# Optimization experiments

Measured on AMD Instinct MI355X. Metric: run time of the kernel, lower is better.

The kernel has to match this reference:

```python
import jax, jax.numpy as jnp
import numpy as np

N_NODES = 50000
N_EDGES = 800000
IN_DIM_N = 256
IN_DIM_E = 64
OUT_DIM_N = 64
OUT_DIM_E = 64


def setup_inputs() -> dict:
    key = jax.random.key(0)
    ks = jax.random.split(key, 8)
    nfeats = jax.random.normal(ks[0], (N_NODES, IN_DIM_N), dtype=jnp.float32)
    efeats = jax.random.normal(ks[1], (N_EDGES, IN_DIM_E), dtype=jnp.float32)
    src = jax.random.randint(ks[2], (N_EDGES,), 0, N_NODES)
    dst = jax.random.randint(ks[3], (N_EDGES,), 0, N_NODES)
    # xavier-style scaled weights
    W_fc = jax.random.normal(ks[4], (OUT_DIM_N, IN_DIM_N), dtype=jnp.float32) * (2.0 / (OUT_DIM_N + IN_DIM_N)) ** 0.5
    cat_dim = IN_DIM_E + 2 * OUT_DIM_N  # 192
    W_e = jax.random.normal(ks[5], (OUT_DIM_E, cat_dim), dtype=jnp.float32) * (2.0 / (OUT_DIM_E + cat_dim)) ** 0.5
    b_e = jnp.zeros((OUT_DIM_E,), dtype=jnp.float32)
    w_c = jax.random.normal(ks[6], (1, OUT_DIM_E), dtype=jnp.float32) * (2.0 / (1 + OUT_DIM_E)) ** 0.5
    return {"nfeats": nfeats, "efeats": efeats, "src": src, "dst": dst,
            "W_fc": W_fc, "W_e": W_e, "b_e": b_e, "w_c": w_c}


def reference(nfeats, efeats, src, dst, W_fc, W_e, b_e, w_c):
    N = nfeats.shape[0]
    # node projection (no bias)
    z = nfeats @ W_fc.T                                   # [N, out_n]
    # edge attention MLP on [z_src | efeat | z_dst]
    stacked = jnp.concatenate([z[src], efeats, z[dst]], axis=1)  # [E, in_e + 2*out_n]
    feat_e = jax.nn.leaky_relu(stacked @ W_e.T + b_e)     # [E, out_e], slope 0.01 = torch default
    a = (feat_e @ w_c.T)[:, 0]                            # [E]
    # segment softmax over incoming edges of each dst node
    m = jax.ops.segment_max(a, dst, num_segments=N)       # [N] (-inf for empty segs, never gathered)
    ex = jnp.exp(a - m[dst])                              # [E]
    s = jax.ops.segment_sum(ex, dst, num_segments=N)      # [N]
    alpha = ex / s[dst]                                   # [E]
    # weighted scatter-sum aggregate of source z
    h = jax.ops.segment_sum(alpha[:, None] * z[src], dst, num_segments=N)  # [N, out_n]
    return h, feat_e
```

## Files before the change

kernel.cpp:

```cpp
#include <hip/hip_runtime.h>
#include <hip/hip_bf16.h>

#define N_NODES 50000
#define N_EDGES 800000
#define IN_N    256
#define D       64

typedef __attribute__((ext_vector_type(8))) short short8;
typedef __attribute__((ext_vector_type(4))) float f32x4;

__device__ __forceinline__ float bf2f(unsigned short h) {
    union { unsigned int u; float f; } x; x.u = ((unsigned int)h) << 16; return x.f;
}
__device__ __forceinline__ unsigned short f2bf(float f) {
    union { float f; unsigned int u; } x; x.f = f;
    unsigned int r = x.u + 0x7fff + ((x.u >> 16) & 1);
    return (unsigned short)(r >> 16);
}
__device__ __forceinline__ short8 pack8(f32x4 p0, f32x4 p1) {
    short8 r;
    r[0] = (short)f2bf(p0[0]); r[1] = (short)f2bf(p0[1]);
    r[2] = (short)f2bf(p0[2]); r[3] = (short)f2bf(p0[3]);
    r[4] = (short)f2bf(p1[0]); r[5] = (short)f2bf(p1[1]);
    r[6] = (short)f2bf(p1[2]); r[7] = (short)f2bf(p1[3]);
    return r;
}

__global__ void count_kernel(const int* __restrict__ dst, int* __restrict__ count) {
    int i = blockIdx.x * blockDim.x + threadIdx.x;
    int stride = gridDim.x * blockDim.x;
    for (; i < N_EDGES / 4; i += stride) {
        int4 d = ((const int4*)dst)[i];
        atomicAdd(&count[d.x], 1);
        atomicAdd(&count[d.y], 1);
        atomicAdd(&count[d.z], 1);
        atomicAdd(&count[d.w], 1);
    }
}

__global__ __launch_bounds__(1024) void scan_kernel(const int* __restrict__ count,
                                                    int* __restrict__ offsets,
                                                    int* __restrict__ cursor) {
    __shared__ int part[1024];
    const int t = threadIdx.x;
    const int C = (N_NODES + 1023) / 1024;
    const int base = t * C;
    int s = 0;
    for (int i = 0; i < C; ++i) {
        int idx = base + i;
        if (idx < N_NODES) s += count[idx];
    }
    part[t] = s;
    __syncthreads();
    for (int st = 1; st < 1024; st <<= 1) {
        int v = (t >= st) ? part[t - st] : 0;
        __syncthreads();
        part[t] += v;
        __syncthreads();
    }
    int run = part[t] - s;
    for (int i = 0; i < C; ++i) {
        int idx = base + i;
        if (idx < N_NODES) {
            offsets[idx] = run;
            cursor[idx]  = run;
            run += count[idx];
        }
    }
    if (t == 1023) offsets[N_NODES] = part[1023];
}

__global__ void prep_kernel(const float* __restrict__ W_fc, const float* __restrict__ W_e,
                            unsigned short* __restrict__ Wz,
                            unsigned short* __restrict__ Wu,
                            unsigned short* __restrict__ Wv)
{
    int flat = blockIdx.x * blockDim.x + threadIdx.x;
    if (flat >= 3 * 64 * 256) return;
    int mat = flat >> 14;
    int idx = flat & 16383;
    if (mat == 0) {
        Wz[idx] = f2bf(W_fc[idx]);
        return;
    }
    int o = idx >> 8, i = idx & 255;
    const float* wrow = W_e + (size_t)o * 192 + (mat == 2 ? 128 : 0);
    float s = 0.f;
    #pragma unroll 8
    for (int j = 0; j < 64; ++j) s += wrow[j] * W_fc[(size_t)j * 256 + i];
    (mat == 1 ? Wu : Wv)[idx] = f2bf(s);
}

__global__ __launch_bounds__(256) void node_kernel(
    const float* __restrict__ nf,
    const unsigned short* __restrict__ Wz, const unsigned short* __restrict__ Wu,
    const unsigned short* __restrict__ Wv, const float* __restrict__ b_e,
    unsigned short* __restrict__ z_bf, unsigned short* __restrict__ u_bf,
    unsigned short* __restrict__ v_bf)
{
    const int lanelo = threadIdx.x & 15, quad = (threadIdx.x >> 4) & 3;
    float bias[4];
    #pragma unroll
    for (int t = 0; t < 4; ++t) bias[t] = b_e[t * 16 + lanelo];
    const int wflat = blockIdx.x * 4 + (threadIdx.x >> 6);
    const int nw = gridDim.x * 4;
    const f32x4 z4 = {0.f, 0.f, 0.f, 0.f};
    for (int g = wflat; g < N_NODES / 16; g += nw) {
        const int n0 = g * 16;
        f32x4 az[4] = {z4, z4, z4, z4};
        f32x4 au[4] = {z4, z4, z4, z4};
        f32x4 av[4] = {z4, z4, z4, z4};
        const float* arow = nf + (size_t)(n0 + lanelo) * IN_N;
        #pragma unroll
        for (int h = 0; h < 8; ++h) {
            const float* ap = arow + h * 32 + quad * 8;
            f32x4 p0 = *(const f32x4*)ap;
            f32x4 p1 = *(const f32x4*)(ap + 4);
            short8 a = pack8(p0, p1);
            const int bo = h * 32 + quad * 8;
            #pragma unroll
            for (int t = 0; t < 4; ++t) {
                const size_t rb = (size_t)(t * 16 + lanelo) * 256 + bo;
                az[t] = __builtin_amdgcn_mfma_f32_16x16x32_bf16(a, *(const short8*)&Wz[rb], az[t], 0, 0, 0);
                au[t] = __builtin_amdgcn_mfma_f32_16x16x32_bf16(a, *(const short8*)&Wu[rb], au[t], 0, 0, 0);
                av[t] = __builtin_amdgcn_mfma_f32_16x16x32_bf16(a, *(const short8*)&Wv[rb], av[t], 0, 0, 0);
            }
        }
        #pragma unroll
        for (int t = 0; t < 4; ++t)
            #pragma unroll
            for (int r = 0; r < 4; ++r) {
                const size_t row = (size_t)(n0 + quad * 4 + r) * D + t * 16 + lanelo;
                z_bf[row] = f2bf(az[t][r]);
                u_bf[row] = f2bf(au[t][r] + bias[t]);
                v_bf[row] = f2bf(av[t][r]);
            }
    }
}

__global__ __launch_bounds__(256) void edge_kernel(
    const float* __restrict__ efeats,
    const int* __restrict__ src, const int* __restrict__ dst,
    const float* __restrict__ W_e, const float* __restrict__ w_c,
    const unsigned short* __restrict__ u_bf, const unsigned short* __restrict__ v_bf,
    int* __restrict__ cursor, unsigned long long* __restrict__ csr,
    float* __restrict__ feat_out)
{
    const int lanelo = threadIdx.x & 15, quad = (threadIdx.x >> 4) & 3;
    short8 b2[4][2];
    #pragma unroll
    for (int t = 0; t < 4; ++t)
        #pragma unroll
        for (int h = 0; h < 2; ++h)
            #pragma unroll
            for (int j = 0; j < 8; ++j)
                b2[t][h][j] = (short)f2bf(W_e[(size_t)(t * 16 + lanelo) * 192 + 64 + h * 32 + quad * 8 + j]);
    float wcv[4];
    #pragma unroll
    for (int t = 0; t < 4; ++t) wcv[t] = w_c[t * 16 + lanelo];

    const int wflat = blockIdx.x * 4 + (threadIdx.x >> 6);
    const int nw = gridDim.x * 4;
    const f32x4 z4 = {0.f, 0.f, 0.f, 0.f};
    for (int g = wflat; g < N_EDGES / 16; g += nw) {
        const int e0 = g * 16;
        f32x4 acc[4] = {z4, z4, z4, z4};
        const float* ar = efeats + (size_t)(e0 + lanelo) * D;
        #pragma unroll
        for (int h = 0; h < 2; ++h) {
            f32x4 p0 = __builtin_nontemporal_load((const f32x4*)(ar + h * 32 + quad * 8));
            f32x4 p1 = __builtin_nontemporal_load((const f32x4*)(ar + h * 32 + quad * 8 + 4));
            short8 a = pack8(p0, p1);
            #pragma unroll
            for (int t = 0; t < 4; ++t)
                acc[t] = __builtin_amdgcn_mfma_f32_16x16x32_bf16(a, b2[t][h], acc[t], 0, 0, 0);
        }
        int sn[4], dn[4];
        #pragma unroll
        for (int r = 0; r < 4; ++r) {
            sn[r] = src[e0 + quad * 4 + r];
            dn[r] = dst[e0 + quad * 4 + r];
        }
        float part[4];
        #pragma unroll
        for (int r = 0; r < 4; ++r) {
            float p = 0.f;
            #pragma unroll
            for (int t = 0; t < 4; ++t) {
                float f = acc[t][r]
                        + bf2f(u_bf[(size_t)sn[r] * D + t * 16 + lanelo])
                        + bf2f(v_bf[(size_t)dn[r] * D + t * 16 + lanelo]);
                f = f > 0.f ? f : 0.01f * f;
                __builtin_nontemporal_store(f, &feat_out[(size_t)(e0 + quad * 4 + r) * D + t * 16 + lanelo]);
                p += f * wcv[t];
            }
            part[r] = p;
        }
        #pragma unroll
        for (int st = 1; st < 16; st <<= 1) {
            #pragma unroll
            for (int r = 0; r < 4; ++r) part[r] += __shfl_xor(part[r], st, 64);
        }
        #pragma unroll
        for (int r = 0; r < 4; ++r) {
            float ex = __expf(part[r]);
            if (lanelo == 0) {
                int pos = atomicAdd(&cursor[dn[r]], 1);
                csr[pos] = ((unsigned long long)__float_as_uint(ex) << 32)
                         | (unsigned long long)(unsigned int)sn[r];
            }
        }
    }
}

__global__ __launch_bounds__(256) void agg_kernel(
    const unsigned long long* __restrict__ csr,
    const int* __restrict__ offsets,
    const unsigned short* __restrict__ z_bf,
    float* __restrict__ h)
{
    const int lane = threadIdx.x & 63;
    const int wid = (blockIdx.x * blockDim.x + threadIdx.x) >> 6;
    const int nw = (gridDim.x * blockDim.x) >> 6;
    for (int n = wid; n < N_NODES; n += nw) {
        const int off = offsets[n];
        const int d = offsets[n + 1] - off;
        float acc = 0.f, ssum = 0.f;
        for (int base = 0; base < d; base += 64) {
            const int cnt = min(d - base, 64);
            unsigned long long pk = csr[off + base + min(lane, cnt - 1)];
            unsigned int hi = (unsigned int)(pk >> 32);
            unsigned int lo = (unsigned int)pk;
            int j = 0;
            for (; j + 4 <= cnt; j += 4) {
                float x0 = __uint_as_float(__shfl((int)hi, j,     64));
                float x1 = __uint_as_float(__shfl((int)hi, j + 1, 64));
                float x2 = __uint_as_float(__shfl((int)hi, j + 2, 64));
                float x3 = __uint_as_float(__shfl((int)hi, j + 3, 64));
                int s0 = __shfl((int)lo, j,     64);
                int s1 = __shfl((int)lo, j + 1, 64);
                int s2 = __shfl((int)lo, j + 2, 64);
                int s3 = __shfl((int)lo, j + 3, 64);
                float z0 = bf2f(z_bf[(size_t)s0 * D + lane]);
                float z1 = bf2f(z_bf[(size_t)s1 * D + lane]);
                float z2 = bf2f(z_bf[(size_t)s2 * D + lane]);
                float z3 = bf2f(z_bf[(size_t)s3 * D + lane]);
                acc += x0 * z0; acc += x1 * z1; acc += x2 * z2; acc += x3 * z3;
                ssum += (x0 + x1) + (x2 + x3);
            }
            for (; j < cnt; ++j) {
                float xj = __uint_as_float(__shfl((int)hi, j, 64));
                int sj = __shfl((int)lo, j, 64);
                acc += xj * bf2f(z_bf[(size_t)sj * D + lane]);
                ssum += xj;
            }
        }
        h[(size_t)n * D + lane] = ssum > 0.f ? acc / ssum : 0.f;
    }
}

extern "C" void kernel_launch(void* const* d_in, const int* in_sizes, int n_in,
                              void* d_out, int out_size, void* d_ws, size_t ws_size,
                              hipStream_t stream)
{
    const float* nfeats = (const float*)d_in[0];
    const float* efeats = (const float*)d_in[1];
    const int* src = (const int*)d_in[2];
    const int* dst = (const int*)d_in[3];
    const float* W_fc = (const float*)d_in[4];
    const float* W_e  = (const float*)d_in[5];
    const float* b_e  = (const float*)d_in[6];
    const float* w_c  = (const float*)d_in[7];

    unsigned short* z_bf = (unsigned short*)d_ws;
    unsigned short* u_bf = z_bf + (size_t)N_NODES * D;
    unsigned short* v_bf = u_bf + (size_t)N_NODES * D;
    unsigned long long* csr = (unsigned long long*)(v_bf + (size_t)N_NODES * D);
    unsigned short* Wz = (unsigned short*)(csr + (size_t)N_EDGES);
    unsigned short* Wu = Wz + 64 * 256;
    unsigned short* Wv = Wu + 64 * 256;
    int* count   = (int*)(Wv + 64 * 256);
    int* offsets = count + N_NODES;
    int* cursor  = offsets + N_NODES + 1;

    float* h_out = (float*)d_out;
    float* f_out = h_out + (size_t)N_NODES * D;

    hipMemsetAsync(count, 0, N_NODES * sizeof(int), stream);
    count_kernel<<<512, 256, 0, stream>>>(dst, count);
    scan_kernel<<<1, 1024, 0, stream>>>(count, offsets, cursor);
    prep_kernel<<<192, 256, 0, stream>>>(W_fc, W_e, Wz, Wu, Wv);
    node_kernel<<<782, 256, 0, stream>>>(nfeats, Wz, Wu, Wv, b_e, z_bf, u_bf, v_bf);
    edge_kernel<<<2048, 256, 0, stream>>>(efeats, src, dst, W_e, w_c, u_bf, v_bf,
                                          cursor, csr, f_out);
    agg_kernel<<<2048, 256, 0, stream>>>(csr, offsets, z_bf, h_out);
}
```

Baseline: 722.3 us.

## Fuse all phases into one cooperative persistent kernel with grid syncs

Replaces the memset and six separate kernel launches with a single cooperative kernel of 1024 blocks that runs zeroing, weight prep, degree count, a hierarchical three-stage scan, node projection, edge MLP, and aggregation, separated by grid-wide barriers. The single-block scan becomes a chunked parallel scan, and the end-exclusive cursor produced by the edge scatter now supplies segment bounds, so the offsets array is gone. The aggregation loop no longer cooperatively loads the CSR into lanes and broadcasts it with shuffles; every lane loads each CSR entry directly, unrolled by eight. The goal is to remove launch gaps and the serial scan. The trade-off is grid-sync overhead, a fixed grid size for every phase, and extra redundant CSR loads in aggregation.

```diff
diff --git a/kernel.cpp b/kernel.cpp
--- a/kernel.cpp
+++ b/kernel.cpp
@@ -1,10 +1,16 @@
 #include <hip/hip_runtime.h>
 #include <hip/hip_bf16.h>
+#include <hip/hip_cooperative_groups.h>
+
+namespace cg = cooperative_groups;
 
 #define N_NODES 50000
 #define N_EDGES 800000
 #define IN_N    256
 #define D       64
+#define NBLK    1024
+#define NTHR    256
+#define NCHUNK  1021
 
 typedef __attribute__((ext_vector_type(8))) short short8;
 typedef __attribute__((ext_vector_type(4))) float f32x4;
@@ -26,10 +32,29 @@
     return r;
 }
 
-__global__ void count_kernel(const int* __restrict__ dst, int* __restrict__ count) {
-    int i = blockIdx.x * blockDim.x + threadIdx.x;
-    int stride = gridDim.x * blockDim.x;
-    for (; i < N_EDGES / 4; i += stride) {
+
+__device__ __forceinline__ void ph_zero_prep(int gtid, int gsz,
+    const float* __restrict__ W_fc, const float* __restrict__ W_e,
+    unsigned short* __restrict__ Wz, unsigned short* __restrict__ Wu,
+    unsigned short* __restrict__ Wv, int* __restrict__ count)
+{
+    for (int i = gtid; i < N_NODES; i += gsz) count[i] = 0;
+    for (int f = gtid; f < 3 * 64 * 256; f += gsz) {
+        int mat = f >> 14, idx = f & 16383;
+        if (mat == 0) { Wz[idx] = f2bf(W_fc[idx]); continue; }
+        int o = idx >> 8, i = idx & 255;
+        const float* wrow = W_e + (size_t)o * 192 + (mat == 2 ? 128 : 0);
+        float s = 0.f;
+        #pragma unroll 8
+        for (int j = 0; j < 64; ++j) s += wrow[j] * W_fc[(size_t)j * 256 + i];
+        (mat == 1 ? Wu : Wv)[idx] = f2bf(s);
+    }
+}
+
+__device__ __forceinline__ void ph_count(int gtid, int gsz,
+    const int* __restrict__ dst, int* __restrict__ count)
+{
+    for (int i = gtid; i < N_EDGES / 4; i += gsz) {
         int4 d = ((const int4*)dst)[i];
         atomicAdd(&count[d.x], 1);
         atomicAdd(&count[d.y], 1);
@@ -38,74 +63,69 @@
     }
 }
 
-__global__ __launch_bounds__(1024) void scan_kernel(const int* __restrict__ count,
-                                                    int* __restrict__ offsets,
-                                                    int* __restrict__ cursor) {
-    __shared__ int part[1024];
-    const int t = threadIdx.x;
-    const int C = (N_NODES + 1023) / 1024;
-    const int base = t * C;
-    int s = 0;
-    for (int i = 0; i < C; ++i) {
-        int idx = base + i;
-        if (idx < N_NODES) s += count[idx];
-    }
-    part[t] = s;
-    __syncthreads();
-    for (int st = 1; st < 1024; st <<= 1) {
-        int v = (t >= st) ? part[t - st] : 0;
-        __syncthreads();
-        part[t] += v;
-        __syncthreads();
-    }
-    int run = part[t] - s;
-    for (int i = 0; i < C; ++i) {
-        int idx = base + i;
-        if (idx < N_NODES) {
-            offsets[idx] = run;
-            cursor[idx]  = run;
-            run += count[idx];
-        }
-    }
-    if (t == 1023) offsets[N_NODES] = part[1023];
-}
-
-__global__ void prep_kernel(const float* __restrict__ W_fc, const float* __restrict__ W_e,
-                            unsigned short* __restrict__ Wz,
-                            unsigned short* __restrict__ Wu,
-                            unsigned short* __restrict__ Wv)
-{
-    int flat = blockIdx.x * blockDim.x + threadIdx.x;
-    if (flat >= 3 * 64 * 256) return;
-    int mat = flat >> 14;
-    int idx = flat & 16383;
-    if (mat == 0) {
-        Wz[idx] = f2bf(W_fc[idx]);
-        return;
-    }
-    int o = idx >> 8, i = idx & 255;
-    const float* wrow = W_e + (size_t)o * 192 + (mat == 2 ? 128 : 0);
-    float s = 0.f;
-    #pragma unroll 8
-    for (int j = 0; j < 64; ++j) s += wrow[j] * W_fc[(size_t)j * 256 + i];
-    (mat == 1 ? Wu : Wv)[idx] = f2bf(s);
-}
-
-__global__ __launch_bounds__(256) void node_kernel(
+__device__ __forceinline__ void ph_scan_a(
+    const int* __restrict__ count, int* __restrict__ cursor, int* __restrict__ partial)
+{
+    int chunk = blockIdx.x;
+    if (chunk >= NCHUNK || threadIdx.x >= 64) return;
+    int lane = threadIdx.x;
+    int idx = chunk * 49 + lane;
+    int val = (lane < 49 && idx < N_NODES) ? count[idx] : 0;
+    int inc = val;
+    #pragma unroll
+    for (int st = 1; st < 64; st <<= 1) {
+        int o = __shfl_up(inc, st, 64);
+        if (lane >= st) inc += o;
+    }
+    if (lane < 49 && idx < N_NODES) cursor[idx] = inc - val;
+    if (lane == 63) partial[chunk] = inc;
+}
+
+__device__ __forceinline__ void ph_scan_b(
+    const int* __restrict__ partial, int* __restrict__ base)
+{
+    if (blockIdx.x != 0 || threadIdx.x >= 64) return;
+    int lane = threadIdx.x;
+    int vals[16]; int s = 0;
+    #pragma unroll
+    for (int k = 0; k < 16; ++k) {
+        int idx = lane * 16 + k;
+        int v = (idx < NCHUNK) ? partial[idx] : 0;
+        vals[k] = v; s += v;
+    }
+    int inc = s;
+    #pragma unroll
+    for (int st = 1; st < 64; st <<= 1) {
+        int o = __shfl_up(inc, st, 64);
+        if (lane >= st) inc += o;
+    }
+    int run = inc - s;
+    #pragma unroll
+    for (int k = 0; k < 16; ++k) {
+        int idx = lane * 16 + k;
+        if (idx < NCHUNK) base[idx] = run;
+        run += vals[k];
+    }
+}
+
+__device__ __forceinline__ void ph_scan_c(int gtid, int gsz,
+    int* __restrict__ cursor, const int* __restrict__ base)
+{
+    for (int i = gtid; i < N_NODES; i += gsz) cursor[i] += base[i / 49];
+}
+
+__device__ __forceinline__ void ph_node(int wv, int nwv, int lanelo, int quad,
     const float* __restrict__ nf,
     const unsigned short* __restrict__ Wz, const unsigned short* __restrict__ Wu,
     const unsigned short* __restrict__ Wv, const float* __restrict__ b_e,
     unsigned short* __restrict__ z_bf, unsigned short* __restrict__ u_bf,
     unsigned short* __restrict__ v_bf)
 {
-    const int lanelo = threadIdx.x & 15, quad = (threadIdx.x >> 4) & 3;
     float bias[4];
     #pragma unroll
     for (int t = 0; t < 4; ++t) bias[t] = b_e[t * 16 + lanelo];
-    const int wflat = blockIdx.x * 4 + (threadIdx.x >> 6);
-    const int nw = gridDim.x * 4;
     const f32x4 z4 = {0.f, 0.f, 0.f, 0.f};
-    for (int g = wflat; g < N_NODES / 16; g += nw) {
+    for (int g = wv; g < N_NODES / 16; g += nwv) {
         const int n0 = g * 16;
         f32x4 az[4] = {z4, z4, z4, z4};
         f32x4 au[4] = {z4, z4, z4, z4};
@@ -138,7 +158,7 @@
     }
 }
 
-__global__ __launch_bounds__(256) void edge_kernel(
+__device__ __forceinline__ void ph_edge(int wv, int nwv, int lanelo, int quad,
     const float* __restrict__ efeats,
     const int* __restrict__ src, const int* __restrict__ dst,
     const float* __restrict__ W_e, const float* __restrict__ w_c,
@@ -146,7 +166,6 @@
     int* __restrict__ cursor, unsigned long long* __restrict__ csr,
     float* __restrict__ feat_out)
 {
-    const int lanelo = threadIdx.x & 15, quad = (threadIdx.x >> 4) & 3;
     short8 b2[4][2];
     #pragma unroll
     for (int t = 0; t < 4; ++t)
@@ -159,10 +178,8 @@
     #pragma unroll
     for (int t = 0; t < 4; ++t) wcv[t] = w_c[t * 16 + lanelo];
 
-    const int wflat = blockIdx.x * 4 + (threadIdx.x >> 6);
-    const int nw = gridDim.x * 4;
     const f32x4 z4 = {0.f, 0.f, 0.f, 0.f};
-    for (int g = wflat; g < N_EDGES / 16; g += nw) {
+    for (int g = wv; g < N_EDGES / 16; g += nwv) {
         const int e0 = g * 16;
         f32x4 acc[4] = {z4, z4, z4, z4};
         const float* ar = efeats + (size_t)(e0 + lanelo) * D;
@@ -213,50 +230,99 @@
     }
 }
 
-__global__ __launch_bounds__(256) void agg_kernel(
-    const unsigned long long* __restrict__ csr,
-    const int* __restrict__ offsets,
-    const unsigned short* __restrict__ z_bf,
-    float* __restrict__ h)
+__device__ __forceinline__ void ph_agg(int wv, int nwv,
+    const unsigned long long* __restrict__ csr, const int* __restrict__ cursor,
+    const unsigned short* __restrict__ z_bf, float* __restrict__ h)
 {
     const int lane = threadIdx.x & 63;
-    const int wid = (blockIdx.x * blockDim.x + threadIdx.x) >> 6;
-    const int nw = (gridDim.x * blockDim.x) >> 6;
-    for (int n = wid; n < N_NODES; n += nw) {
-        const int off = offsets[n];
-        const int d = offsets[n + 1] - off;
+    for (int n = wv; n < N_NODES; n += nwv) {
+        int beg = (n == 0) ? 0 : cursor[n - 1];
+        int end = cursor[n];
         float acc = 0.f, ssum = 0.f;
-        for (int base = 0; base < d; base += 64) {
-            const int cnt = min(d - base, 64);
-            unsigned long long pk = csr[off + base + min(lane, cnt - 1)];
-            unsigned int hi = (unsigned int)(pk >> 32);
-            unsigned int lo = (unsigned int)pk;
-            int j = 0;
-            for (; j + 4 <= cnt; j += 4) {
-                float x0 = __uint_as_float(__shfl((int)hi, j,     64));
-                float x1 = __uint_as_float(__shfl((int)hi, j + 1, 64));
-                float x2 = __uint_as_float(__shfl((int)hi, j + 2, 64));
-                float x3 = __uint_as_float(__shfl((int)hi, j + 3, 64));
-                int s0 = __shfl((int)lo, j,     64);
-                int s1 = __shfl((int)lo, j + 1, 64);
-                int s2 = __shfl((int)lo, j + 2, 64);
-                int s3 = __shfl((int)lo, j + 3, 64);
-                float z0 = bf2f(z_bf[(size_t)s0 * D + lane]);
-                float z1 = bf2f(z_bf[(size_t)s1 * D + lane]);
-                float z2 = bf2f(z_bf[(size_t)s2 * D + lane]);
-                float z3 = bf2f(z_bf[(size_t)s3 * D + lane]);
-                acc += x0 * z0; acc += x1 * z1; acc += x2 * z2; acc += x3 * z3;
-                ssum += (x0 + x1) + (x2 + x3);
-            }
-            for (; j < cnt; ++j) {
-                float xj = __uint_as_float(__shfl((int)hi, j, 64));
-                int sj = __shfl((int)lo, j, 64);
-                acc += xj * bf2f(z_bf[(size_t)sj * D + lane]);
-                ssum += xj;
-            }
-        }
-        h[(size_t)n * D + lane] = ssum > 0.f ? acc / ssum : 0.f;
-    }
+        for (int j = beg; j < end; j += 8) {
+            #pragma unroll
+            for (int k = 0; k < 8; ++k) {
+                int jj = j + k;
+                if (jj < end) {
+                    unsigned long long p = csr[jj];
+                    float x = __uint_as_float((unsigned int)(p >> 32));
+                    int sidx = (int)(p & 0xffffffffu);
+                    acc += x * bf2f(z_bf[(size_t)sidx * D + lane]);
+                    ssum += x;
+                }
+            }
+        }
+        __builtin_nontemporal_store(ssum > 0.f ? acc / ssum : 0.f, &h[(size_t)n * D + lane]);
+    }
+}
+
+
+__global__ void __launch_bounds__(NTHR, 4) fused_all(
+    const float* nfeats, const float* efeats, const int* src, const int* dst,
+    const float* W_fc, const float* W_e, const float* b_e, const float* w_c,
+    unsigned short* z_bf, unsigned short* u_bf, unsigned short* v_bf,
+    unsigned long long* csr, unsigned short* Wz, unsigned short* Wu, unsigned short* Wv,
+    int* count, int* cursor, int* partial, int* baseArr,
+    float* h_out, float* f_out)
+{
+    cg::grid_group grid = cg::this_grid();
+    const int gtid = blockIdx.x * NTHR + threadIdx.x;
+    const int gsz  = gridDim.x * NTHR;
+    const int wv = gtid >> 6, nwv = gsz >> 6;
+    const int lanelo = threadIdx.x & 15, quad = (threadIdx.x >> 4) & 3;
+
+    ph_zero_prep(gtid, gsz, W_fc, W_e, Wz, Wu, Wv, count);
+    grid.sync();
+    ph_count(gtid, gsz, dst, count);
+    grid.sync();
+    ph_scan_a(count, cursor, partial);
+    grid.sync();
+    ph_scan_b(partial, baseArr);
+    grid.sync();
+    ph_scan_c(gtid, gsz, cursor, baseArr);
+    ph_node(wv, nwv, lanelo, quad, nfeats, Wz, Wu, Wv, b_e, z_bf, u_bf, v_bf);
+    grid.sync();
+    ph_edge(wv, nwv, lanelo, quad, efeats, src, dst, W_e, w_c, u_bf, v_bf,
+            cursor, csr, f_out);
+    grid.sync();
+    ph_agg(wv, nwv, csr, cursor, z_bf, h_out);
+}
+
+
+__global__ void __launch_bounds__(NTHR) k_zero_prep(const float* W_fc, const float* W_e,
+    unsigned short* Wz, unsigned short* Wu, unsigned short* Wv, int* count) {
+    ph_zero_prep(blockIdx.x * NTHR + threadIdx.x, gridDim.x * NTHR, W_fc, W_e, Wz, Wu, Wv, count);
+}
+__global__ void __launch_bounds__(NTHR) k_count(const int* dst, int* count) {
+    ph_count(blockIdx.x * NTHR + threadIdx.x, gridDim.x * NTHR, dst, count);
+}
+__global__ void __launch_bounds__(NTHR) k_scan_a(const int* count, int* cursor, int* partial) {
+    ph_scan_a(count, cursor, partial);
+}
+__global__ void __launch_bounds__(NTHR) k_scan_b(const int* partial, int* base) {
+    ph_scan_b(partial, base);
+}
+__global__ void __launch_bounds__(NTHR) k_scan_c(int* cursor, const int* base) {
+    ph_scan_c(blockIdx.x * NTHR + threadIdx.x, gridDim.x * NTHR, cursor, base);
+}
+__global__ void __launch_bounds__(NTHR) k_node(const float* nf,
+    const unsigned short* Wz, const unsigned short* Wu, const unsigned short* Wv,
+    const float* b_e, unsigned short* z_bf, unsigned short* u_bf, unsigned short* v_bf) {
+    int gtid = blockIdx.x * NTHR + threadIdx.x;
+    ph_node(gtid >> 6, (gridDim.x * NTHR) >> 6, threadIdx.x & 15, (threadIdx.x >> 4) & 3,
+            nf, Wz, Wu, Wv, b_e, z_bf, u_bf, v_bf);
+}
+__global__ void __launch_bounds__(NTHR) k_edge(const float* efeats, const int* src, const int* dst,
+    const float* W_e, const float* w_c, const unsigned short* u_bf, const unsigned short* v_bf,
+    int* cursor, unsigned long long* csr, float* feat_out) {
+    int gtid = blockIdx.x * NTHR + threadIdx.x;
+    ph_edge(gtid >> 6, (gridDim.x * NTHR) >> 6, threadIdx.x & 15, (threadIdx.x >> 4) & 3,
+            efeats, src, dst, W_e, w_c, u_bf, v_bf, cursor, csr, feat_out);
+}
+__global__ void __launch_bounds__(NTHR) k_agg(const unsigned long long* csr, const int* cursor,
+    const unsigned short* z_bf, float* h) {
+    int gtid = blockIdx.x * NTHR + threadIdx.x;
+    ph_agg(gtid >> 6, (gridDim.x * NTHR) >> 6, csr, cursor, z_bf, h);
 }
 
 extern "C" void kernel_launch(void* const* d_in, const int* in_sizes, int n_in,
@@ -280,18 +346,32 @@
     unsigned short* Wu = Wz + 64 * 256;
     unsigned short* Wv = Wu + 64 * 256;
     int* count   = (int*)(Wv + 64 * 256);
-    int* offsets = count + N_NODES;
-    int* cursor  = offsets + N_NODES + 1;
+    int* cursor  = count + N_NODES;
+    int* partial = cursor + N_NODES;
+    int* baseArr = partial + NCHUNK;
 
     float* h_out = (float*)d_out;
     float* f_out = h_out + (size_t)N_NODES * D;
 
-    hipMemsetAsync(count, 0, N_NODES * sizeof(int), stream);
-    count_kernel<<<512, 256, 0, stream>>>(dst, count);
-    scan_kernel<<<1, 1024, 0, stream>>>(count, offsets, cursor);
-    prep_kernel<<<192, 256, 0, stream>>>(W_fc, W_e, Wz, Wu, Wv);
-    node_kernel<<<782, 256, 0, stream>>>(nfeats, Wz, Wu, Wv, b_e, z_bf, u_bf, v_bf);
-    edge_kernel<<<2048, 256, 0, stream>>>(efeats, src, dst, W_e, w_c, u_bf, v_bf,
+    void* args[] = {
+        (void*)&nfeats, (void*)&efeats, (void*)&src, (void*)&dst,
+        (void*)&W_fc, (void*)&W_e, (void*)&b_e, (void*)&w_c,
+        (void*)&z_bf, (void*)&u_bf, (void*)&v_bf, (void*)&csr,
+        (void*)&Wz, (void*)&Wu, (void*)&Wv,
+        (void*)&count, (void*)&cursor, (void*)&partial, (void*)&baseArr,
+        (void*)&h_out, (void*)&f_out
+    };
+    hipError_t err = hipLaunchCooperativeKernel((void*)fused_all,
+        dim3(NBLK), dim3(NTHR), args, 0, stream);
+    if (err != hipSuccess) {
+        k_zero_prep<<<NBLK, NTHR, 0, stream>>>(W_fc, W_e, Wz, Wu, Wv, count);
+        k_count<<<NBLK, NTHR, 0, stream>>>(dst, count);
+        k_scan_a<<<NBLK, NTHR, 0, stream>>>(count, cursor, partial);
+        k_scan_b<<<1, NTHR, 0, stream>>>(partial, baseArr);
+        k_scan_c<<<NBLK, NTHR, 0, stream>>>(cursor, baseArr);
+        k_node<<<NBLK, NTHR, 0, stream>>>(nfeats, Wz, Wu, Wv, b_e, z_bf, u_bf, v_bf);
+        k_edge<<<2048, NTHR, 0, stream>>>(efeats, src, dst, W_e, w_c, u_bf, v_bf,
                                           cursor, csr, f_out);
-    agg_kernel<<<2048, 256, 0, stream>>>(csr, offsets, z_bf, h_out);
-}
+        k_agg<<<2048, NTHR, 0, stream>>>(csr, cursor, z_bf, h_out);
+    }
+}
```

New measurement: 1.451 ms. 2.01x slower.
